# Kernel optimization log

Hardware: AMD Instinct MI355X
Metric: run time of the kernel (lower is better)

Reference implementation:

```python
import jax, jax.numpy as jnp
import numpy as np

N = 100000   # total nodes
E = 600000   # total edges
G = 2048     # graphs in batch
DIN = 9      # input node feature dim
D = 128      # hidden == output dim
L = 5        # GIN layers
BN_EPS = 1e-5
LN_EPS = 1e-5


def setup_inputs() -> dict:
    key = jax.random.key(0)
    ks = jax.random.split(key, 24)
    s = 0.05
    x = jax.random.normal(ks[0], (N, DIN), jnp.float32)
    edge_index = jax.random.randint(ks[1], (2, E), 0, N, dtype=jnp.int32)
    batch = jnp.sort(jax.random.randint(ks[2], (N,), 0, G, dtype=jnp.int32))
    return {
        "x": x,
        "edge_index": edge_index,
        "batch": batch,
        # node embedding
        "node_emb_W": jax.random.normal(ks[3], (DIN, D), jnp.float32) * s,
        "node_emb_b": jnp.zeros((D,), jnp.float32),
        # GIN layer MLPs, stacked over layers: Linear(D,2D) -> ReLU -> Linear(2D,D)
        "W1s": jax.random.normal(ks[4], (L, D, 2 * D), jnp.float32) * s,
        "b1s": jnp.zeros((L, 2 * D), jnp.float32),
        "W2s": jax.random.normal(ks[5], (L, 2 * D, D), jnp.float32) * s,
        "b2s": jnp.zeros((L, D), jnp.float32),
        # BatchNorm affine params per layer
        "bn_g": jnp.ones((L, D), jnp.float32),
        "bn_b": jnp.zeros((L, D), jnp.float32),
        # virtual node
        "vn_emb": jax.random.normal(ks[6], (1, D), jnp.float32),
        "vn_W1": jax.random.normal(ks[7], (D, D), jnp.float32) * s,
        "vn_b1": jnp.zeros((D,), jnp.float32),
        "vn_W2": jax.random.normal(ks[8], (D, D), jnp.float32) * s,
        "vn_b2": jnp.zeros((D,), jnp.float32),
        # graph MLP: Linear -> LayerNorm -> ReLU -> Linear
        "gm_W1": jax.random.normal(ks[9], (D, D), jnp.float32) * s,
        "gm_b1": jnp.zeros((D,), jnp.float32),
        "ln_g": jnp.ones((D,), jnp.float32),
        "ln_b": jnp.zeros((D,), jnp.float32),
        "gm_W2": jax.random.normal(ks[10], (D, D), jnp.float32) * s,
        "gm_b2": jnp.zeros((D,), jnp.float32),
    }


def _mean_pool(h, batch):
    # segment mean over graphs: [N, D] -> [G, D]
    s = jax.ops.segment_sum(h, batch, num_segments=G)
    cnt = jax.ops.segment_sum(jnp.ones((h.shape[0], 1), h.dtype), batch, num_segments=G)
    return s / jnp.maximum(cnt, 1.0)


def _batchnorm(m, g, b):
    mu = jnp.mean(m, axis=0)
    var = jnp.mean(jnp.square(m - mu), axis=0)  # biased var (torch train-mode norm)
    return (m - mu) * jax.lax.rsqrt(var + BN_EPS) * g + b


def reference(x, edge_index, batch, node_emb_W, node_emb_b, W1s, b1s, W2s, b2s,
              bn_g, bn_b, vn_emb, vn_W1, vn_b1, vn_W2, vn_b2,
              gm_W1, gm_b1, ln_g, ln_b, gm_W2, gm_b2):
    src, dst = edge_index[0], edge_index[1]
    h = x @ node_emb_W + node_emb_b                       # [N, D]
    vn = jnp.tile(vn_emb, (G, 1))                         # [G, D]
    for i in range(L):
        h_prev = h
        # GINConv (eps=0): mlp(h + sum_{j->i} h_j) via gather/scatter-add
        agg = jax.ops.segment_sum(h[src], dst, num_segments=N)
        m = h + agg
        m = jax.nn.relu(m @ W1s[i] + b1s[i]) @ W2s[i] + b2s[i]
        h = jax.nn.relu(_batchnorm(m, bn_g[i], bn_b[i]))
        # (dropout is identity in eval mode)
        if i > 0:
            h = h + h_prev
        # virtual node: pool -> MLP -> broadcast back
        temp = _mean_pool(h, batch)                       # [G, D]
        vn = vn + (jax.nn.relu(temp @ vn_W1 + vn_b1) @ vn_W2 + vn_b2)
        h = h + vn[batch]
    node_features = h                                     # output_projection = Identity
    gf = _mean_pool(node_features, batch)                 # [G, D]
    gf = gf @ gm_W1 + gm_b1
    mu = jnp.mean(gf, axis=-1, keepdims=True)
    var = jnp.mean(jnp.square(gf - mu), axis=-1, keepdims=True)
    gf = (gf - mu) * jax.lax.rsqrt(var + LN_EPS) * ln_g + ln_b
    gf = jax.nn.relu(gf)
    graph_features = gf @ gm_W2 + gm_b2
    return node_features, graph_features
```

## Files before the change

### kernel.cpp

```cpp
#include <hip/hip_runtime.h>
#include <stdint.h>

#define NNODES 100000
#define NEDGES 600000
#define NGRAPH 2048
#define DD 128
#define NLAYER 5
#define NPAD 100096
#define SCAN_NB 391
#define NSTAT 32

typedef __attribute__((ext_vector_type(8))) __bf16 bf16x8;
typedef __attribute__((ext_vector_type(4))) float f32x4;
typedef __attribute__((ext_vector_type(8))) ushort u16x8;

__device__ __forceinline__ ushort f2b(float f) {
    union { float f; uint32_t u; } v; v.f = f;
    uint32_t r = v.u + 0x7FFFu + ((v.u >> 16) & 1u);
    return (ushort)(r >> 16);
}

__device__ __forceinline__ float b2f(ushort u) {
    union { uint32_t u; float f; } v; v.u = ((uint32_t)u) << 16; return v.f;
}

__device__ __forceinline__ void gload_lds16(const void* g, void* l) {
    __builtin_amdgcn_global_load_lds(
        (const __attribute__((address_space(1))) void*)g,
        (__attribute__((address_space(3))) void*)l, 16, 0, 0);
}

__global__ void prep_w_kernel(const float* __restrict__ W1s, const float* __restrict__ W2s,
                              ushort* __restrict__ w1t, ushort* __restrict__ w2t) {
    int idx = blockIdx.x * 256 + threadIdx.x;
    const int per = 128 * 256;
    if (idx < NLAYER * per) {
        int i = idx / per, rem = idx % per;
        int n = rem >> 7, k = rem & 127;
        w1t[idx] = f2b(W1s[(size_t)i * per + k * 256 + n]);
    } else if (idx < 2 * NLAYER * per) {
        int j = idx - NLAYER * per;
        int i = j / per, rem = j % per;
        int n = rem >> 8, k = rem & 255;
        w2t[j] = f2b(W2s[(size_t)i * per + k * 128 + n]);
    }
}

__global__ void node_embed_kernel(const float* __restrict__ x, const float* __restrict__ W,
                                  const float* __restrict__ b, ushort* __restrict__ hb,
                                  const float* __restrict__ vne, float* __restrict__ vn) {
    int idx = blockIdx.x * 256 + threadIdx.x;
    if (idx < NNODES * 128) {
        int n = idx >> 7, d = idx & 127;
        float v = b[d];
#pragma unroll
        for (int k = 0; k < 9; ++k) v += x[n * 9 + k] * W[k * 128 + d];
        hb[(size_t)n * 128 + d] = f2b(v);
    } else if (idx < NNODES * 128 + NGRAPH * 128) {
        int r = idx - NNODES * 128;
        vn[r] = vne[r & 127];
    }
}


__global__ void deg_kernel(const int* __restrict__ dst, int* __restrict__ deg) {
    int e = blockIdx.x * 256 + threadIdx.x;
    if (e < NEDGES) atomicAdd(&deg[dst[e]], 1);
}

__global__ void scan_part_kernel(const int* __restrict__ deg, int* __restrict__ partials) {
    int i = blockIdx.x * 256 + threadIdx.x;
    int lane = threadIdx.x & 63, w = threadIdx.x >> 6;
    int v = (i < NNODES) ? deg[i] : 0;
#pragma unroll
    for (int o = 1; o < 64; o <<= 1) v += __shfl_xor(v, o);
    __shared__ int ws[4];
    if (lane == 0) ws[w] = v;
    __syncthreads();
    if (threadIdx.x == 0) partials[blockIdx.x] = ws[0] + ws[1] + ws[2] + ws[3];
}

__global__ __launch_bounds__(512)
void scan_top_kernel(int* __restrict__ partials) {
    __shared__ int s[512];
    int t = threadIdx.x;
    int v = (t < SCAN_NB) ? partials[t] : 0;
    s[t] = v;
    __syncthreads();
#pragma unroll
    for (int o = 1; o < 512; o <<= 1) {
        int n = (t >= o) ? s[t - o] : 0;
        __syncthreads();
        s[t] += n;
        __syncthreads();
    }
    if (t < SCAN_NB) partials[t] = s[t] - v;
}

__global__ void scan_blocks_kernel(const int* __restrict__ deg, const int* __restrict__ partials,
                                   int* __restrict__ rs, int* __restrict__ cursor) {
    int i = blockIdx.x * 256 + threadIdx.x;
    int lane = threadIdx.x & 63, w = threadIdx.x >> 6;
    int v = (i < NNODES) ? deg[i] : 0;
    int x = v;
#pragma unroll
    for (int o = 1; o < 64; o <<= 1) {
        int n = __shfl_up(x, o);
        if (lane >= o) x += n;
    }
    __shared__ int ws[4];
    if (lane == 63) ws[w] = x;
    __syncthreads();
    if (threadIdx.x == 0) {
        int a = 0;
#pragma unroll
        for (int k = 0; k < 4; ++k) { int t = ws[k]; ws[k] = a; a += t; }
    }
    __syncthreads();
    int excl = (x - v) + ws[w] + partials[blockIdx.x];
    if (i < NNODES) { rs[i] = excl; cursor[i] = excl; }
    if (i == 0) rs[NNODES] = NEDGES;
}

__global__ void csr_scatter_kernel(const int* __restrict__ src, const int* __restrict__ dst,
                                   int* __restrict__ cursor, int* __restrict__ csrc) {
    int e = blockIdx.x * 256 + threadIdx.x;
    if (e < NEDGES) {
        int p = atomicAdd(&cursor[dst[e]], 1);
        csrc[p] = src[e];
    }
}

__device__ __forceinline__ int lbound(const int* __restrict__ b, int key) {
    int lo = 0, hi = NNODES;
    while (lo < hi) { int m = (lo + hi) >> 1; if (b[m] < key) lo = m + 1; else hi = m; }
    return lo;
}

__global__ void gstart_kernel(const int* __restrict__ batch, int* __restrict__ gstart,
                              float* __restrict__ inv) {
    int g = blockIdx.x * 256 + threadIdx.x;
    if (g <= NGRAPH)
        gstart[g] = (g == NGRAPH) ? NNODES : lbound(batch, g);
    if (g < NGRAPH) {
        int c = lbound(batch, g + 1) - lbound(batch, g);
        inv[g] = 1.f / (float)(c > 0 ? c : 1);
    }
}


__global__ __launch_bounds__(256)
void gin_agg_kernel(const ushort* __restrict__ hb, const int* __restrict__ rs,
                    const int* __restrict__ csrc, ushort* __restrict__ xb) {
    int slot = threadIdx.x >> 4;
    int j = threadIdx.x & 15;
    int node = blockIdx.x * 16 + slot;
    if (node >= NNODES) return;
    int s = rs[node], e = rs[node + 1];
    u16x8 v0 = *(const u16x8*)(hb + (size_t)node * 128 + j * 8);
    float a[8], b[8];
#pragma unroll
    for (int t = 0; t < 8; ++t) { a[t] = b2f(v0[t]); b[t] = 0.f; }
    int k = s;
    for (; k + 1 < e; k += 2) {
        int s0 = csrc[k], s1 = csrc[k + 1];
        u16x8 va = *(const u16x8*)(hb + (size_t)s0 * 128 + j * 8);
        u16x8 vb = *(const u16x8*)(hb + (size_t)s1 * 128 + j * 8);
#pragma unroll
        for (int t = 0; t < 8; ++t) { a[t] += b2f(va[t]); b[t] += b2f(vb[t]); }
    }
    if (k < e) {
        int s0 = csrc[k];
        u16x8 va = *(const u16x8*)(hb + (size_t)s0 * 128 + j * 8);
#pragma unroll
        for (int t = 0; t < 8; ++t) a[t] += b2f(va[t]);
    }
    u16x8 o;
#pragma unroll
    for (int t = 0; t < 8; ++t) o[t] = f2b(a[t] + b[t]);
    *(u16x8*)(xb + (size_t)node * 128 + j * 8) = o;
}

#define MLP_TILES 4
#define MLP_GRID 391
__global__ __launch_bounds__(256, 2)
void fused_mlp_kernel(const ushort* __restrict__ A, const ushort* __restrict__ W1,
                      const float* __restrict__ b1, const ushort* __restrict__ W2,
                      const float* __restrict__ b2, ushort* __restrict__ out_b,
                      float* __restrict__ stats) {
    __shared__ __align__(16) ushort lA[8192];
    __shared__ __align__(16) ushort mid[16384];
    const int tid = threadIdx.x;
    const int lane = tid & 63, w = tid >> 6;
    const int q = lane >> 4, l16 = lane & 15;
    float* sbase = stats + (blockIdx.x & (NSTAT - 1)) * 256;

    bf16x8 w1f[4][4], w2f[8][2];
#pragma unroll
    for (int ks = 0; ks < 4; ++ks)
#pragma unroll
        for (int ni = 0; ni < 4; ++ni)
            w1f[ks][ni] = *(const bf16x8*)(W1 + (size_t)(w * 64 + ni * 16 + l16) * 128 + ks * 32 + q * 8);
#pragma unroll
    for (int ks = 0; ks < 8; ++ks)
#pragma unroll
        for (int ni = 0; ni < 2; ++ni)
            w2f[ks][ni] = *(const bf16x8*)(W2 + (size_t)(w * 32 + ni * 16 + l16) * 256 + ks * 32 + q * 8);

    {
        int rb = blockIdx.x * (64 * MLP_TILES);
#pragma unroll
        for (int p = 0; p < 4; ++p)
            gload_lds16(A + (size_t)(rb + lane) * 128 + p * 32 + w * 8,
                        &lA[(size_t)(p * 256 + w * 64 + lane) * 8]);
    }

    for (int tt = 0; tt < MLP_TILES; ++tt) {
        const int rb = blockIdx.x * (64 * MLP_TILES) + tt * 64;
        __syncthreads();

        f32x4 acc1[4][4] = {};
#pragma unroll
        for (int ks = 0; ks < 4; ++ks) {
            bf16x8 af[4];
#pragma unroll
            for (int mi = 0; mi < 4; ++mi)
                af[mi] = *(const bf16x8*)&lA[ks * 2048 + q * 512 + (mi * 16 + l16) * 8];
#pragma unroll
            for (int mi = 0; mi < 4; ++mi)
#pragma unroll
                for (int ni = 0; ni < 4; ++ni)
                    acc1[mi][ni] = __builtin_amdgcn_mfma_f32_16x16x32_bf16(af[mi], w1f[ks][ni], acc1[mi][ni], 0, 0, 0);
        }

#pragma unroll
        for (int ni = 0; ni < 4; ++ni) {
            int col = w * 64 + ni * 16 + l16;
            float bs = b1[col];
            int g2 = col >> 3, jj = col & 7;
#pragma unroll
            for (int mi = 0; mi < 4; ++mi) {
                int rowb = mi * 16 + q * 4;
#pragma unroll
                for (int r = 0; r < 4; ++r) {
                    float v = acc1[mi][ni][r] + bs;
                    v = v > 0.f ? v : 0.f;
                    mid[g2 * 512 + (rowb + r) * 8 + jj] = f2b(v);
                }
            }
        }
        __syncthreads();

        if (tt + 1 < MLP_TILES) {
            int rb2 = rb + 64;
#pragma unroll
            for (int p = 0; p < 4; ++p)
                gload_lds16(A + (size_t)(rb2 + lane) * 128 + p * 32 + w * 8,
                            &lA[(size_t)(p * 256 + w * 64 + lane) * 8]);
        }

        f32x4 acc2[4][2] = {};
#pragma unroll
        for (int ks = 0; ks < 8; ++ks) {
            bf16x8 af[4];
#pragma unroll
            for (int mi = 0; mi < 4; ++mi)
                af[mi] = *(const bf16x8*)&mid[(ks * 4 + q) * 512 + (mi * 16 + l16) * 8];
#pragma unroll
            for (int mi = 0; mi < 4; ++mi)
#pragma unroll
                for (int ni = 0; ni < 2; ++ni)
                    acc2[mi][ni] = __builtin_amdgcn_mfma_f32_16x16x32_bf16(af[mi], w2f[ks][ni], acc2[mi][ni], 0, 0, 0);
        }

#pragma unroll
        for (int ni = 0; ni < 2; ++ni) {
            int col = w * 32 + ni * 16 + l16;
            float bs = b2[col];
            float s = 0.f, sq = 0.f;
#pragma unroll
            for (int mi = 0; mi < 4; ++mi) {
                int row = rb + mi * 16 + q * 4;
#pragma unroll
                for (int r = 0; r < 4; ++r) {
                    float v = acc2[mi][ni][r] + bs;
                    out_b[(size_t)(row + r) * 128 + col] = f2b(v);
                    if (row + r < NNODES) { s += v; sq += v * v; }
                }
            }
            s  += __shfl_xor(s, 16);  s  += __shfl_xor(s, 32);
            sq += __shfl_xor(sq, 16); sq += __shfl_xor(sq, 32);
            if (lane < 16) {
                atomicAdd(&sbase[col], s);
                atomicAdd(&sbase[128 + col], sq);
            }
        }
    }
}

__global__ __launch_bounds__(512)
void bn_apply_kernel(const ushort* __restrict__ m, const float* __restrict__ stats,
                     const float* __restrict__ bng, const float* __restrict__ bnb,
                     ushort* __restrict__ hb, int resid) {
    __shared__ float sC[128], sS[128];
    if (threadIdx.x < 128) {
        int d = threadIdx.x;
        float sum = 0.f, sq = 0.f;
#pragma unroll
        for (int c = 0; c < NSTAT; ++c) {
            sum += stats[c * 256 + d];
            sq  += stats[c * 256 + 128 + d];
        }
        float mu = sum * (1.f / NNODES);
        float var = sq * (1.f / NNODES) - mu * mu;
        var = var < 0.f ? 0.f : var;
        float sc = bng[d] * rsqrtf(var + 1e-5f);
        sC[d] = sc;
        sS[d] = bnb[d] - mu * sc;
    }
    __syncthreads();
    int t = blockIdx.x * 512 + threadIdx.x;
    if (t >= NNODES * 16) return;
    int row = t >> 4, j = t & 15;
    u16x8 mu8 = *(const u16x8*)(m + (size_t)row * 128 + j * 8);
    float wv[8];
#pragma unroll
    for (int k = 0; k < 8; ++k)
        wv[k] = fmaxf(b2f(mu8[k]) * sC[j * 8 + k] + sS[j * 8 + k], 0.f);
    if (resid) {
        u16x8 hp = *(const u16x8*)(hb + (size_t)row * 128 + j * 8);
#pragma unroll
        for (int k = 0; k < 8; ++k) wv[k] += b2f(hp[k]);
    }
    u16x8 o;
#pragma unroll
    for (int k = 0; k < 8; ++k) o[k] = f2b(wv[k]);
    *(u16x8*)(hb + (size_t)row * 128 + j * 8) = o;
}

__global__ void vn_update_kernel(const ushort* __restrict__ hb, const int* __restrict__ gstart,
                                 const float* __restrict__ inv,
                                 const float* __restrict__ W1, const float* __restrict__ b1,
                                 const float* __restrict__ W2, const float* __restrict__ b2,
                                 float* __restrict__ vn, float* __restrict__ stats) {
    __shared__ float t[128], t1[128];
    int g = blockIdx.x, d = threadIdx.x;
    int s = gstart[g], e = gstart[g + 1];
    float acc = 0.f;
    for (int r = s; r < e; ++r) acc += b2f(hb[(size_t)r * 128 + d]);
    t[d] = acc * inv[g];
    if (g < NSTAT) { stats[g * 256 + d] = 0.f; stats[g * 256 + 128 + d] = 0.f; }
    __syncthreads();
    float a = b1[d];
    for (int k = 0; k < 128; ++k) a += t[k] * W1[k * 128 + d];
    t1[d] = fmaxf(a, 0.f);
    __syncthreads();
    float o = b2[d];
    for (int k = 0; k < 128; ++k) o += t1[k] * W2[k * 128 + d];
    vn[g * 128 + d] += o;
}

template<int FINAL>
__global__ __launch_bounds__(512)
void add_vn_kernel(ushort* __restrict__ hb, const float* __restrict__ vn,
                   const int* __restrict__ batch, float* __restrict__ outN) {
    int t = blockIdx.x * 512 + threadIdx.x;
    if (t >= NNODES * 16) return;
    int row = t >> 4, j = t & 15;
    int g = batch[row];
    float4 v0 = ((const float4*)(vn + (size_t)g * 128))[j * 2];
    float4 v1 = ((const float4*)(vn + (size_t)g * 128))[j * 2 + 1];
    u16x8 hv = *(const u16x8*)(hb + (size_t)row * 128 + j * 8);
    float wv[8];
    wv[0] = b2f(hv[0]) + v0.x; wv[1] = b2f(hv[1]) + v0.y;
    wv[2] = b2f(hv[2]) + v0.z; wv[3] = b2f(hv[3]) + v0.w;
    wv[4] = b2f(hv[4]) + v1.x; wv[5] = b2f(hv[5]) + v1.y;
    wv[6] = b2f(hv[6]) + v1.z; wv[7] = b2f(hv[7]) + v1.w;
    if (FINAL) {
        float4* op = (float4*)(outN + (size_t)row * 128 + j * 8);
        op[0] = make_float4(wv[0], wv[1], wv[2], wv[3]);
        op[1] = make_float4(wv[4], wv[5], wv[6], wv[7]);
    } else {
        u16x8 o;
#pragma unroll
        for (int k = 0; k < 8; ++k) o[k] = f2b(wv[k]);
        *(u16x8*)(hb + (size_t)row * 128 + j * 8) = o;
    }
}

__global__ void graph_mlp_kernel(const ushort* __restrict__ hb, const int* __restrict__ gstart,
                                 const float* __restrict__ inv, const float* __restrict__ vn,
                                 const float* __restrict__ W1, const float* __restrict__ b1,
                                 const float* __restrict__ lng, const float* __restrict__ lnb,
                                 const float* __restrict__ W2, const float* __restrict__ b2,
                                 float* __restrict__ out) {
    __shared__ float t[128], t1[128], red[2];
    int g = blockIdx.x, d = threadIdx.x;
    int lane = d & 63, w = d >> 6;
    int s = gstart[g], e = gstart[g + 1];
    float acc = 0.f;
    for (int r = s; r < e; ++r) acc += b2f(hb[(size_t)r * 128 + d]);
    t[d] = (e > s) ? (acc * inv[g] + vn[(size_t)g * 128 + d]) : 0.f;
    __syncthreads();
    float a = b1[d];
    for (int k = 0; k < 128; ++k) a += t[k] * W1[k * 128 + d];
    float ssum = a;
#pragma unroll
    for (int o = 1; o < 64; o <<= 1) ssum += __shfl_xor(ssum, o);
    if (lane == 0) red[w] = ssum;
    __syncthreads();
    float mu = (red[0] + red[1]) * (1.f / 128.f);
    float dv = a - mu;
    float qq = dv * dv;
#pragma unroll
    for (int o = 1; o < 64; o <<= 1) qq += __shfl_xor(qq, o);
    __syncthreads();
    if (lane == 0) red[w] = qq;
    __syncthreads();
    float var = (red[0] + red[1]) * (1.f / 128.f);
    float v = dv * rsqrtf(var + 1e-5f) * lng[d] + lnb[d];
    v = fmaxf(v, 0.f);
    t1[d] = v;
    __syncthreads();
    float o2 = b2[d];
    for (int k = 0; k < 128; ++k) o2 += t1[k] * W2[k * 128 + d];
    out[g * 128 + d] = o2;
}

extern "C" void kernel_launch(void* const* d_in, const int* in_sizes, int n_in,
                              void* d_out, int out_size, void* d_ws, size_t ws_size,
                              hipStream_t stream) {
    const float* x    = (const float*)d_in[0];
    const int*   edge = (const int*)d_in[1];
    const int*   src  = edge;
    const int*   dst  = edge + NEDGES;
    const int*   batch = (const int*)d_in[2];
    const float* nW   = (const float*)d_in[3];
    const float* nb   = (const float*)d_in[4];
    const float* W1s  = (const float*)d_in[5];
    const float* b1s  = (const float*)d_in[6];
    const float* W2s  = (const float*)d_in[7];
    const float* b2s  = (const float*)d_in[8];
    const float* bng  = (const float*)d_in[9];
    const float* bnb  = (const float*)d_in[10];
    const float* vne  = (const float*)d_in[11];
    const float* vW1  = (const float*)d_in[12];
    const float* vb1  = (const float*)d_in[13];
    const float* vW2  = (const float*)d_in[14];
    const float* vb2  = (const float*)d_in[15];
    const float* gW1  = (const float*)d_in[16];
    const float* gb1  = (const float*)d_in[17];
    const float* lng  = (const float*)d_in[18];
    const float* lnb  = (const float*)d_in[19];
    const float* gW2  = (const float*)d_in[20];
    const float* gb2  = (const float*)d_in[21];

    char* ws = (char*)d_ws;
    auto alloc = [&](size_t bytes) { char* p = ws; ws += (bytes + 255) & ~(size_t)255; return p; };
    float*  stats = (float*)alloc((size_t)NSTAT * 256 * 4);
    ushort* hb    = (ushort*)alloc((size_t)NPAD * 128 * 2);
    ushort* mbuf  = (ushort*)alloc((size_t)NPAD * 128 * 2);
    ushort* xb    = (ushort*)alloc((size_t)NPAD * 128 * 2);
    float*  vn    = (float*)alloc((size_t)NGRAPH * 128 * 4);
    ushort* w1t   = (ushort*)alloc((size_t)NLAYER * 256 * 128 * 2);
    ushort* w2t   = (ushort*)alloc((size_t)NLAYER * 128 * 256 * 2);
    float*  inv   = (float*)alloc((size_t)NGRAPH * 4);
    int*    gstart= (int*)alloc((size_t)(NGRAPH + 1) * 4);
    int*    deg   = (int*)alloc((size_t)NNODES * 4);
    int*    rs    = (int*)alloc((size_t)(NNODES + 1) * 4);
    int*    cursor= (int*)alloc((size_t)NNODES * 4);
    int*    csrc  = (int*)alloc((size_t)NEDGES * 4);
    int*    partials = (int*)alloc((size_t)SCAN_NB * 4);

    float* outN = (float*)d_out;
    float* outG = outN + (size_t)NNODES * 128;

    hipMemsetAsync(stats, 0, (size_t)NSTAT * 256 * 4, stream);
    hipMemsetAsync(deg, 0, (size_t)NNODES * 4, stream);

    deg_kernel<<<(NEDGES + 255) / 256, 256, 0, stream>>>(dst, deg);
    scan_part_kernel<<<SCAN_NB, 256, 0, stream>>>(deg, partials);
    scan_top_kernel<<<1, 512, 0, stream>>>(partials);
    scan_blocks_kernel<<<SCAN_NB, 256, 0, stream>>>(deg, partials, rs, cursor);
    csr_scatter_kernel<<<(NEDGES + 255) / 256, 256, 0, stream>>>(src, dst, cursor, csrc);
    gstart_kernel<<<(NGRAPH + 256) / 256, 256, 0, stream>>>(batch, gstart, inv);

    prep_w_kernel<<<(2 * NLAYER * 128 * 256 + 255) / 256, 256, 0, stream>>>(W1s, W2s, w1t, w2t);
    node_embed_kernel<<<((NNODES + NGRAPH) * 128 + 255) / 256, 256, 0, stream>>>(
        x, nW, nb, hb, vne, vn);

    const int flatNB = (NNODES * 16 + 511) / 512;
    for (int i = 0; i < NLAYER; ++i) {
        gin_agg_kernel<<<(NNODES + 15) / 16, 256, 0, stream>>>(hb, rs, csrc, xb);
        fused_mlp_kernel<<<MLP_GRID, 256, 0, stream>>>(
            xb, w1t + (size_t)i * 256 * 128, b1s + i * 256,
            w2t + (size_t)i * 128 * 256, b2s + i * 128, mbuf, stats);
        bn_apply_kernel<<<flatNB, 512, 0, stream>>>(
            mbuf, stats, bng + i * 128, bnb + i * 128, hb, i > 0 ? 1 : 0);
        vn_update_kernel<<<NGRAPH, 128, 0, stream>>>(hb, gstart, inv, vW1, vb1, vW2, vb2, vn, stats);
        if (i < NLAYER - 1)
            add_vn_kernel<0><<<flatNB, 512, 0, stream>>>(hb, vn, batch, nullptr);
        else
            add_vn_kernel<1><<<flatNB, 512, 0, stream>>>(hb, vn, batch, outN);
    }
    graph_mlp_kernel<<<NGRAPH, 128, 0, stream>>>(hb, gstart, inv, vn, gW1, gb1, lng, lnb, gW2, gb2, outG);
}
```

Before: 697.3 us.

## Fuse BatchNorm apply with virtual-node add; compute VN pooling from pre-BN output

The virtual-node update now recomputes BN+ReLU+residual on the fly from the MLP output while pooling per graph. This lets the BN apply and the VN broadcast-add merge into one elementwise pass, removing one full read/write of the node feature buffer per layer. Stats zeroing moves into the aggregation kernel, and the gather loop is unrolled by four for more loads in flight. The trade-off is that the pooling kernel reads two arrays per row and recomputes BN. The final graph pooling uses the updated hb directly instead of adding vn back.

```diff
diff --git a/kernel.cpp b/kernel.cpp
--- a/kernel.cpp
+++ b/kernel.cpp
@@ -151,7 +151,9 @@
 
 __global__ __launch_bounds__(256)
 void gin_agg_kernel(const ushort* __restrict__ hb, const int* __restrict__ rs,
-                    const int* __restrict__ csrc, ushort* __restrict__ xb) {
+                    const int* __restrict__ csrc, ushort* __restrict__ xb,
+                    float* __restrict__ stats) {
+    if (blockIdx.x < NSTAT) stats[blockIdx.x * 256 + threadIdx.x] = 0.f;
     int slot = threadIdx.x >> 4;
     int j = threadIdx.x & 15;
     int node = blockIdx.x * 16 + slot;
@@ -162,14 +164,19 @@
 #pragma unroll
     for (int t = 0; t < 8; ++t) { a[t] = b2f(v0[t]); b[t] = 0.f; }
     int k = s;
-    for (; k + 1 < e; k += 2) {
-        int s0 = csrc[k], s1 = csrc[k + 1];
+    for (; k + 3 < e; k += 4) {
+        int s0 = csrc[k], s1 = csrc[k + 1], s2 = csrc[k + 2], s3 = csrc[k + 3];
         u16x8 va = *(const u16x8*)(hb + (size_t)s0 * 128 + j * 8);
         u16x8 vb = *(const u16x8*)(hb + (size_t)s1 * 128 + j * 8);
-#pragma unroll
-        for (int t = 0; t < 8; ++t) { a[t] += b2f(va[t]); b[t] += b2f(vb[t]); }
-    }
-    if (k < e) {
+        u16x8 vc = *(const u16x8*)(hb + (size_t)s2 * 128 + j * 8);
+        u16x8 vd = *(const u16x8*)(hb + (size_t)s3 * 128 + j * 8);
+#pragma unroll
+        for (int t = 0; t < 8; ++t) {
+            a[t] += b2f(va[t]) + b2f(vc[t]);
+            b[t] += b2f(vb[t]) + b2f(vd[t]);
+        }
+    }
+    for (; k < e; ++k) {
         int s0 = csrc[k];
         u16x8 va = *(const u16x8*)(hb + (size_t)s0 * 128 + j * 8);
 #pragma unroll
@@ -298,10 +305,51 @@
     }
 }
 
+__global__ void vn_update_kernel(const ushort* __restrict__ m, const ushort* __restrict__ hb,
+                                 const float* __restrict__ stats,
+                                 const float* __restrict__ bng, const float* __restrict__ bnb,
+                                 const int* __restrict__ gstart, const float* __restrict__ inv,
+                                 const float* __restrict__ W1, const float* __restrict__ b1,
+                                 const float* __restrict__ W2, const float* __restrict__ b2,
+                                 float* __restrict__ vn, int resid) {
+    __shared__ float t[128], t1[128];
+    int g = blockIdx.x, d = threadIdx.x;
+    float sum = 0.f, sq = 0.f;
+#pragma unroll
+    for (int c = 0; c < NSTAT; ++c) {
+        sum += stats[c * 256 + d];
+        sq  += stats[c * 256 + 128 + d];
+    }
+    float mu = sum * (1.f / NNODES);
+    float var = sq * (1.f / NNODES) - mu * mu;
+    var = var < 0.f ? 0.f : var;
+    float sc = bng[d] * rsqrtf(var + 1e-5f);
+    float sh = bnb[d] - mu * sc;
+
+    int s = gstart[g], e = gstart[g + 1];
+    float acc = 0.f;
+    for (int r = s; r < e; ++r) {
+        float v = fmaxf(b2f(m[(size_t)r * 128 + d]) * sc + sh, 0.f);
+        if (resid) v += b2f(hb[(size_t)r * 128 + d]);
+        acc += v;
+    }
+    t[d] = acc * inv[g];
+    __syncthreads();
+    float a = b1[d];
+    for (int k = 0; k < 128; ++k) a += t[k] * W1[k * 128 + d];
+    t1[d] = fmaxf(a, 0.f);
+    __syncthreads();
+    float o = b2[d];
+    for (int k = 0; k < 128; ++k) o += t1[k] * W2[k * 128 + d];
+    vn[g * 128 + d] += o;
+}
+
+template<int FINAL>
 __global__ __launch_bounds__(512)
-void bn_apply_kernel(const ushort* __restrict__ m, const float* __restrict__ stats,
-                     const float* __restrict__ bng, const float* __restrict__ bnb,
-                     ushort* __restrict__ hb, int resid) {
+void bn_vn_apply_kernel(const ushort* __restrict__ m, const float* __restrict__ stats,
+                        const float* __restrict__ bng, const float* __restrict__ bnb,
+                        const float* __restrict__ vn, const int* __restrict__ batch,
+                        ushort* __restrict__ hb, float* __restrict__ outN, int resid) {
     __shared__ float sC[128], sS[128];
     if (threadIdx.x < 128) {
         int d = threadIdx.x;
@@ -322,74 +370,33 @@
     int t = blockIdx.x * 512 + threadIdx.x;
     if (t >= NNODES * 16) return;
     int row = t >> 4, j = t & 15;
-    u16x8 mu8 = *(const u16x8*)(m + (size_t)row * 128 + j * 8);
-    float wv[8];
-#pragma unroll
-    for (int k = 0; k < 8; ++k)
-        wv[k] = fmaxf(b2f(mu8[k]) * sC[j * 8 + k] + sS[j * 8 + k], 0.f);
-    if (resid) {
-        u16x8 hp = *(const u16x8*)(hb + (size_t)row * 128 + j * 8);
-#pragma unroll
-        for (int k = 0; k < 8; ++k) wv[k] += b2f(hp[k]);
-    }
-    u16x8 o;
-#pragma unroll
-    for (int k = 0; k < 8; ++k) o[k] = f2b(wv[k]);
-    *(u16x8*)(hb + (size_t)row * 128 + j * 8) = o;
-}
-
-__global__ void vn_update_kernel(const ushort* __restrict__ hb, const int* __restrict__ gstart,
-                                 const float* __restrict__ inv,
-                                 const float* __restrict__ W1, const float* __restrict__ b1,
-                                 const float* __restrict__ W2, const float* __restrict__ b2,
-                                 float* __restrict__ vn, float* __restrict__ stats) {
-    __shared__ float t[128], t1[128];
-    int g = blockIdx.x, d = threadIdx.x;
-    int s = gstart[g], e = gstart[g + 1];
-    float acc = 0.f;
-    for (int r = s; r < e; ++r) acc += b2f(hb[(size_t)r * 128 + d]);
-    t[d] = acc * inv[g];
-    if (g < NSTAT) { stats[g * 256 + d] = 0.f; stats[g * 256 + 128 + d] = 0.f; }
-    __syncthreads();
-    float a = b1[d];
-    for (int k = 0; k < 128; ++k) a += t[k] * W1[k * 128 + d];
-    t1[d] = fmaxf(a, 0.f);
-    __syncthreads();
-    float o = b2[d];
-    for (int k = 0; k < 128; ++k) o += t1[k] * W2[k * 128 + d];
-    vn[g * 128 + d] += o;
-}
-
-template<int FINAL>
-__global__ __launch_bounds__(512)
-void add_vn_kernel(ushort* __restrict__ hb, const float* __restrict__ vn,
-                   const int* __restrict__ batch, float* __restrict__ outN) {
-    int t = blockIdx.x * 512 + threadIdx.x;
-    if (t >= NNODES * 16) return;
-    int row = t >> 4, j = t & 15;
     int g = batch[row];
     float4 v0 = ((const float4*)(vn + (size_t)g * 128))[j * 2];
     float4 v1 = ((const float4*)(vn + (size_t)g * 128))[j * 2 + 1];
-    u16x8 hv = *(const u16x8*)(hb + (size_t)row * 128 + j * 8);
+    float vg[8] = {v0.x, v0.y, v0.z, v0.w, v1.x, v1.y, v1.z, v1.w};
+    u16x8 mu8 = *(const u16x8*)(m + (size_t)row * 128 + j * 8);
     float wv[8];
-    wv[0] = b2f(hv[0]) + v0.x; wv[1] = b2f(hv[1]) + v0.y;
-    wv[2] = b2f(hv[2]) + v0.z; wv[3] = b2f(hv[3]) + v0.w;
-    wv[4] = b2f(hv[4]) + v1.x; wv[5] = b2f(hv[5]) + v1.y;
-    wv[6] = b2f(hv[6]) + v1.z; wv[7] = b2f(hv[7]) + v1.w;
+#pragma unroll
+    for (int k = 0; k < 8; ++k)
+        wv[k] = fmaxf(b2f(mu8[k]) * sC[j * 8 + k] + sS[j * 8 + k], 0.f) + vg[k];
+    if (resid) {
+        u16x8 hp = *(const u16x8*)(hb + (size_t)row * 128 + j * 8);
+#pragma unroll
+        for (int k = 0; k < 8; ++k) wv[k] += b2f(hp[k]);
+    }
+    u16x8 o;
+#pragma unroll
+    for (int k = 0; k < 8; ++k) o[k] = f2b(wv[k]);
+    *(u16x8*)(hb + (size_t)row * 128 + j * 8) = o;
     if (FINAL) {
         float4* op = (float4*)(outN + (size_t)row * 128 + j * 8);
         op[0] = make_float4(wv[0], wv[1], wv[2], wv[3]);
         op[1] = make_float4(wv[4], wv[5], wv[6], wv[7]);
-    } else {
-        u16x8 o;
-#pragma unroll
-        for (int k = 0; k < 8; ++k) o[k] = f2b(wv[k]);
-        *(u16x8*)(hb + (size_t)row * 128 + j * 8) = o;
     }
 }
 
 __global__ void graph_mlp_kernel(const ushort* __restrict__ hb, const int* __restrict__ gstart,
-                                 const float* __restrict__ inv, const float* __restrict__ vn,
+                                 const float* __restrict__ inv,
                                  const float* __restrict__ W1, const float* __restrict__ b1,
                                  const float* __restrict__ lng, const float* __restrict__ lnb,
                                  const float* __restrict__ W2, const float* __restrict__ b2,
@@ -400,7 +407,7 @@
     int s = gstart[g], e = gstart[g + 1];
     float acc = 0.f;
     for (int r = s; r < e; ++r) acc += b2f(hb[(size_t)r * 128 + d]);
-    t[d] = (e > s) ? (acc * inv[g] + vn[(size_t)g * 128 + d]) : 0.f;
+    t[d] = acc * inv[g];
     __syncthreads();
     float a = b1[d];
     for (int k = 0; k < 128; ++k) a += t[k] * W1[k * 128 + d];
@@ -491,17 +498,19 @@
 
     const int flatNB = (NNODES * 16 + 511) / 512;
     for (int i = 0; i < NLAYER; ++i) {
-        gin_agg_kernel<<<(NNODES + 15) / 16, 256, 0, stream>>>(hb, rs, csrc, xb);
+        gin_agg_kernel<<<(NNODES + 15) / 16, 256, 0, stream>>>(hb, rs, csrc, xb, stats);
         fused_mlp_kernel<<<MLP_GRID, 256, 0, stream>>>(
             xb, w1t + (size_t)i * 256 * 128, b1s + i * 256,
             w2t + (size_t)i * 128 * 256, b2s + i * 128, mbuf, stats);
-        bn_apply_kernel<<<flatNB, 512, 0, stream>>>(
-            mbuf, stats, bng + i * 128, bnb + i * 128, hb, i > 0 ? 1 : 0);
-        vn_update_kernel<<<NGRAPH, 128, 0, stream>>>(hb, gstart, inv, vW1, vb1, vW2, vb2, vn, stats);
+        vn_update_kernel<<<NGRAPH, 128, 0, stream>>>(
+            mbuf, hb, stats, bng + i * 128, bnb + i * 128, gstart, inv,
+            vW1, vb1, vW2, vb2, vn, i > 0 ? 1 : 0);
         if (i < NLAYER - 1)
-            add_vn_kernel<0><<<flatNB, 512, 0, stream>>>(hb, vn, batch, nullptr);
+            bn_vn_apply_kernel<0><<<flatNB, 512, 0, stream>>>(
+                mbuf, stats, bng + i * 128, bnb + i * 128, vn, batch, hb, nullptr, i > 0 ? 1 : 0);
         else
-            add_vn_kernel<1><<<flatNB, 512, 0, stream>>>(hb, vn, batch, outN);
-    }
-    graph_mlp_kernel<<<NGRAPH, 128, 0, stream>>>(hb, gstart, inv, vn, gW1, gb1, lng, lnb, gW2, gb2, outG);
-}
+            bn_vn_apply_kernel<1><<<flatNB, 512, 0, stream>>>(
+                mbuf, stats, bng + i * 128, bnb + i * 128, vn, batch, hb, outN, 1);
+    }
+    graph_mlp_kernel<<<NGRAPH, 128, 0, stream>>>(hb, gstart, inv, gW1, gb1, lng, lnb, gW2, gb2, outG);
+}
```

New measurement: 742.4 us. 1.06x slower.
